# Optimization experiments

Measured on AMD Instinct MI355X. Metric: run time of the kernel, lower is better.

Reference implementation:

```python
import jax, jax.numpy as jnp
import numpy as np

B, S, D = 4, 2048, 2048
E = 64           # num_experts
TOPK = 2         # num_experts_per_token


def setup_inputs() -> dict:
    key = jax.random.key(0)
    k1, k2, k3 = jax.random.split(key, 3)
    x_real = jax.random.normal(k1, (B, S, D), dtype=jnp.float32)
    x_imag = jax.random.normal(k2, (B, S, D), dtype=jnp.float32)
    # flax Dense: kernel [in_features, out_features] with lecun_normal-ish scale
    W = jax.random.normal(k3, (2 * D, E), dtype=jnp.float32) / np.sqrt(2.0 * D)
    b = jnp.zeros((E,), dtype=jnp.float32)
    return {"x_real": x_real, "x_imag": x_imag, "W": W, "b": b}


def reference(x_real, x_imag, W, b):
    # amp = |x|, phase = angle(x) for x = x_real + i*x_imag
    amp = jnp.hypot(x_real, x_imag)                 # [B,S,D]
    phase = jnp.arctan2(x_imag, x_real)             # [B,S,D]
    routing_input = jnp.concatenate([amp, phase], axis=-1)  # [B,S,2D]
    scores = jnp.einsum('bsf,fe->bse', routing_input, W) + b  # [B,S,E]
    probs = jax.nn.softmax(scores, axis=-1)
    top_k_probs, top_k_indices = jax.lax.top_k(probs, TOPK)   # [B,S,K]
    top_k_probs = top_k_probs / jnp.sum(top_k_probs, axis=-1, keepdims=True)
    return (top_k_probs, top_k_indices)
```

## Files before the change

### kernel.cpp

```cpp
#include <hip/hip_runtime.h>
#include <math.h>

#define NTOK 8192
#define DD   2048
#define EE   64
#define STRIP 16
#define NKH 8
#define DSLICE (DD/NKH)
#define NCH (DSLICE/32)
#define PROB_N (NTOK*2)
#define F_SSTRIDE (128*4*64*8)

typedef __bf16 bf16x8 __attribute__((ext_vector_type(8)));
typedef float  f32x4  __attribute__((ext_vector_type(4)));
typedef unsigned int u32x4 __attribute__((ext_vector_type(4)));

__device__ __forceinline__ void tsplit3(float x, unsigned short& h1,
                                        unsigned short& h2, unsigned short& h3) {
    const unsigned u = __builtin_bit_cast(unsigned, x);
    h1 = (unsigned short)(u >> 16);
    const float f1 = __builtin_bit_cast(float, u & 0xFFFF0000u);
    const float r1 = x - f1;
    const unsigned v = __builtin_bit_cast(unsigned, r1);
    h2 = (unsigned short)(v >> 16);
    const float f2 = __builtin_bit_cast(float, v & 0xFFFF0000u);
    const float r2 = r1 - f2;
    h3 = (unsigned short)(__builtin_bit_cast(unsigned, r2) >> 16);
}

__device__ __forceinline__ float fast_atan2f(float y, float x) {
    const float ax = __builtin_fabsf(x), ay = __builtin_fabsf(y);
    const float hi = fmaxf(ax, ay), lo = fminf(ax, ay);
    const bool  big = lo > 0.4142135679721832f * hi;
    const float num = big ? (lo - hi) : lo;
    const float den = big ? (lo + hi) : hi;
    float rc = __builtin_amdgcn_rcpf(den);
    rc = rc * fmaf(-den, rc, 2.0f);
    const float z  = num * rc;
    const float z2 = z * z;
    float p = fmaf(z2, 8.05374449538e-2f, -1.38776856032e-1f);
    p = fmaf(z2, p, 1.99777106478e-1f);
    p = fmaf(z2, p, -3.33329491539e-1f);
    float r = fmaf(z * z2, p, z);
    r = r + (big ? 0.78539816339744830962f : 0.0f);
    r = (ay > ax) ? (1.57079632679489661923f - r) : r;
    r = (x < 0.0f) ? (3.14159265358979323846f - r) : r;
    return copysignf(r, y);
}

__device__ __forceinline__ unsigned packhi(float a, float b) {
    return __builtin_amdgcn_perm(__builtin_bit_cast(unsigned, b),
                                 __builtin_bit_cast(unsigned, a), 0x07060302u);
}

__device__ __forceinline__ void split_planes(const float* v, bf16x8& o1,
                                             bf16x8& o2, bf16x8& o3) {
    u32x4 P1, P2, P3;
    #pragma unroll
    for (int p = 0; p < 4; ++p) {
        const float a = v[2 * p], b = v[2 * p + 1];
        const float f1a = __builtin_bit_cast(float, __builtin_bit_cast(unsigned, a) & 0xFFFF0000u);
        const float f1b = __builtin_bit_cast(float, __builtin_bit_cast(unsigned, b) & 0xFFFF0000u);
        const float r1a = a - f1a, r1b = b - f1b;
        const float f2a = __builtin_bit_cast(float, __builtin_bit_cast(unsigned, r1a) & 0xFFFF0000u);
        const float f2b = __builtin_bit_cast(float, __builtin_bit_cast(unsigned, r1b) & 0xFFFF0000u);
        const float r2a = r1a - f2a, r2b = r1b - f2b;
        P1[p] = packhi(a, b);
        P2[p] = packhi(r1a, r1b);
        P3[p] = packhi(r2a, r2b);
    }
    o1 = __builtin_bit_cast(bf16x8, P1);
    o2 = __builtin_bit_cast(bf16x8, P2);
    o3 = __builtin_bit_cast(bf16x8, P3);
}

__global__ __launch_bounds__(256) void wsplit(const float* __restrict__ W,
                                              unsigned short* __restrict__ F) {
    const int g  = blockIdx.x * 256 + threadIdx.x;
    const int e  = g & 63;
    const int q  = g >> 6;
    const int d0 = q * 4;
    const int nt = e >> 4;
    const int k  = d0 & 31;
    const int lane = (k >> 3) * 16 + (e & 15);
    const int j0 = k & 7;
    const int ck = 2 * (d0 >> 5);

    unsigned short ah[3][4], ph[3][4];
    #pragma unroll
    for (int i = 0; i < 4; ++i) {
        tsplit3(W[(size_t)(d0 + i) * EE + e],      ah[0][i], ah[1][i], ah[2][i]);
        tsplit3(W[(size_t)(DD + d0 + i) * EE + e], ph[0][i], ph[1][i], ph[2][i]);
    }
    #pragma unroll
    for (int s = 0; s < 3; ++s) {
        ushort4 va = make_ushort4(ah[s][0], ah[s][1], ah[s][2], ah[s][3]);
        ushort4 vp = make_ushort4(ph[s][0], ph[s][1], ph[s][2], ph[s][3]);
        *(ushort4*)&F[(size_t)(((s * 128 + ck)     * 4 + nt) * 64 + lane) * 8 + j0] = va;
        *(ushort4*)&F[(size_t)(((s * 128 + ck + 1) * 4 + nt) * 64 + lane) * 8 + j0] = vp;
    }
}

__global__ __launch_bounds__(512, 4) void gemm_topk(
    const float* __restrict__ xr, const float* __restrict__ xi,
    const unsigned short* __restrict__ F, const float* __restrict__ bias,
    float* __restrict__ out)
{
    __shared__ float score8[NKH][STRIP][EE];
    __shared__ float scoreF[STRIP][EE];

    const int tid  = threadIdx.x;
    const int wv   = tid >> 6;
    const int lane = tid & 63;
    const int fm   = lane & 15;
    const int fq   = lane >> 4;
    const int t0   = blockIdx.x * STRIP;

    const float* prx = xr + (size_t)(t0 + fm) * DD + wv * DSLICE + fq * 8;
    const float* pix = xi + (size_t)(t0 + fm) * DD + wv * DSLICE + fq * 8;
    const unsigned short* bs0 = F + (size_t)(wv * NCH * 2) * 4 * 512 + lane * 8;
    const unsigned short* bs1 = bs0 + F_SSTRIDE;
    const unsigned short* bs2 = bs0 + 2 * F_SSTRIDE;

    f32x4 acc[4];
    #pragma unroll
    for (int n = 0; n < 4; ++n) acc[n] = (f32x4){0.f, 0.f, 0.f, 0.f};

    float4 cr0 = *(const float4*)(prx);
    float4 cr1 = *(const float4*)(prx + 4);
    float4 ci0 = *(const float4*)(pix);
    float4 ci1 = *(const float4*)(pix + 4);
    prx += 32; pix += 32;

    #pragma unroll 2
    for (int c = 0; c < NCH; ++c) {
        float4 nr0, nr1, ni0, ni1;
        if (c + 1 < NCH) {
            nr0 = *(const float4*)(prx);
            nr1 = *(const float4*)(prx + 4);
            ni0 = *(const float4*)(pix);
            ni1 = *(const float4*)(pix + 4);
            prx += 32; pix += 32;
        } else {
            nr0 = cr0; nr1 = cr1; ni0 = ci0; ni1 = ci1;
        }

        const float ar[8] = {cr0.x, cr0.y, cr0.z, cr0.w, cr1.x, cr1.y, cr1.z, cr1.w};
        const float ai[8] = {ci0.x, ci0.y, ci0.z, ci0.w, ci1.x, ci1.y, ci1.z, ci1.w};

        {
            bf16x8 b1[4], b2[4], b3[4];
            #pragma unroll
            for (int n = 0; n < 4; ++n) {
                b1[n] = *(const bf16x8*)(bs0 + n * 512);
                b2[n] = *(const bf16x8*)(bs1 + n * 512);
                b3[n] = *(const bf16x8*)(bs2 + n * 512);
            }
            float av[8];
            #pragma unroll
            for (int j = 0; j < 8; ++j)
                av[j] = sqrtf(fmaf(ar[j], ar[j], ai[j] * ai[j]));
            bf16x8 a1, a2, a3;
            split_planes(av, a1, a2, a3);
            #pragma unroll
            for (int n = 0; n < 4; ++n) {
                acc[n] = __builtin_amdgcn_mfma_f32_16x16x32_bf16(a1, b1[n], acc[n], 0, 0, 0);
                acc[n] = __builtin_amdgcn_mfma_f32_16x16x32_bf16(a1, b2[n], acc[n], 0, 0, 0);
                acc[n] = __builtin_amdgcn_mfma_f32_16x16x32_bf16(a2, b1[n], acc[n], 0, 0, 0);
                acc[n] = __builtin_amdgcn_mfma_f32_16x16x32_bf16(a1, b3[n], acc[n], 0, 0, 0);
                acc[n] = __builtin_amdgcn_mfma_f32_16x16x32_bf16(a2, b2[n], acc[n], 0, 0, 0);
                acc[n] = __builtin_amdgcn_mfma_f32_16x16x32_bf16(a3, b1[n], acc[n], 0, 0, 0);
            }
        }
        {
            bf16x8 b1[4], b2[4], b3[4];
            #pragma unroll
            for (int n = 0; n < 4; ++n) {
                b1[n] = *(const bf16x8*)(bs0 + (4 + n) * 512);
                b2[n] = *(const bf16x8*)(bs1 + (4 + n) * 512);
                b3[n] = *(const bf16x8*)(bs2 + (4 + n) * 512);
            }
            float pv[8];
            #pragma unroll
            for (int j = 0; j < 8; ++j)
                pv[j] = fast_atan2f(ai[j], ar[j]);
            bf16x8 a1, a2, a3;
            split_planes(pv, a1, a2, a3);
            #pragma unroll
            for (int n = 0; n < 4; ++n) {
                acc[n] = __builtin_amdgcn_mfma_f32_16x16x32_bf16(a1, b1[n], acc[n], 0, 0, 0);
                acc[n] = __builtin_amdgcn_mfma_f32_16x16x32_bf16(a1, b2[n], acc[n], 0, 0, 0);
                acc[n] = __builtin_amdgcn_mfma_f32_16x16x32_bf16(a2, b1[n], acc[n], 0, 0, 0);
                acc[n] = __builtin_amdgcn_mfma_f32_16x16x32_bf16(a1, b3[n], acc[n], 0, 0, 0);
                acc[n] = __builtin_amdgcn_mfma_f32_16x16x32_bf16(a2, b2[n], acc[n], 0, 0, 0);
                acc[n] = __builtin_amdgcn_mfma_f32_16x16x32_bf16(a3, b1[n], acc[n], 0, 0, 0);
            }
        }
        bs0 += 8 * 512; bs1 += 8 * 512; bs2 += 8 * 512;
        cr0 = nr0; cr1 = nr1; ci0 = ni0; ci1 = ni1;
    }

    #pragma unroll
    for (int n = 0; n < 4; ++n)
        #pragma unroll
        for (int r = 0; r < 4; ++r)
            score8[wv][fq * 4 + r][n * 16 + fm] = acc[n][r];
    __syncthreads();

    #pragma unroll
    for (int rep = 0; rep < 2; ++rep) {
        const int p = tid + rep * 512;
        const int tok = p >> 6, e = p & 63;
        float s = bias[e];
        #pragma unroll
        for (int w = 0; w < NKH; ++w) s += score8[w][tok][e];
        scoreF[tok][e] = s;
    }
    __syncthreads();

    #pragma unroll
    for (int rep = 0; rep < 2; ++rep) {
        const int tok = wv + rep * 8;
        float v1 = scoreF[tok][lane], v2 = -INFINITY;
        int   i1 = lane, i2 = 64;
        #pragma unroll
        for (int off = 1; off < 64; off <<= 1) {
            const float ov1 = __shfl_xor(v1, off, 64);
            const int   oi1 = __shfl_xor(i1, off, 64);
            const float ov2 = __shfl_xor(v2, off, 64);
            const int   oi2 = __shfl_xor(i2, off, 64);
            const bool b1 = (ov1 > v1) || (ov1 == v1 && oi1 < i1);
            const float n1 = b1 ? ov1 : v1;  const int ni1 = b1 ? oi1 : i1;
            const float c1 = b1 ? v1  : ov1; const int ci1 = b1 ? i1  : oi1;
            const float c2 = b1 ? ov2 : v2;  const int ci2 = b1 ? oi2 : i2;
            const bool b2 = (c1 > c2) || (c1 == c2 && ci1 < ci2);
            v1 = n1; i1 = ni1;
            v2 = b2 ? c1 : c2; i2 = b2 ? ci1 : ci2;
        }
        if (lane == 0) {
            const int t = t0 + tok;
            const float z  = expf(v2 - v1);
            const float p1 = 1.0f / (1.0f + z);
            const float p2 = z / (1.0f + z);
            out[(size_t)t * 2 + 0] = p1;
            out[(size_t)t * 2 + 1] = p2;
            out[PROB_N + (size_t)t * 2 + 0] = (float)i1;
            out[PROB_N + (size_t)t * 2 + 1] = (float)i2;
        }
    }
}

extern "C" void kernel_launch(void* const* d_in, const int* in_sizes, int n_in,
                              void* d_out, int out_size, void* d_ws, size_t ws_size,
                              hipStream_t stream) {
    const float* xr = (const float*)d_in[0];
    const float* xi = (const float*)d_in[1];
    const float* W  = (const float*)d_in[2];
    const float* b  = (const float*)d_in[3];
    float* out = (float*)d_out;
    unsigned short* F = (unsigned short*)d_ws;

    wsplit<<<128, 256, 0, stream>>>(W, F);
    gemm_topk<<<NTOK / STRIP, 512, 0, stream>>>(xr, xi, F, b, out);
}
```

Measured before the change: 187.6 us.

## Split K across two blocks per token strip with atomic score reduction

The GEMM kernel now splits the feature dimension across two blocks per 16-token strip, which doubles the grid and raises the occupancy hint. Partial scores are combined with global atomicAdd into a zeroed workspace buffer. A separate finalize kernel then does the top-2 softmax selection. The inner loop also drops the register double-buffering of x loads and interleaves the B fragment loads with the MFMAs. The aim is more parallelism and latency hiding, at the cost of an extra launch, atomic traffic and an 8192x64 score round-trip through memory.

After: 196.9 us. 1.05x slower.

```diff
diff --git a/kernel.cpp b/kernel.cpp
--- a/kernel.cpp
+++ b/kernel.cpp
@@ -4,10 +4,11 @@
 #define NTOK 8192
 #define DD   2048
 #define EE   64
-#define STRIP 16
-#define NKH 8
-#define DSLICE (DD/NKH)
-#define NCH (DSLICE/32)
+#define TSTRIP 16
+#define NKW 8
+#define KSPL 2
+#define DW 128
+#define NCH (DW/32)
 #define PROB_N (NTOK*2)
 #define F_SSTRIDE (128*4*64*8)
 
@@ -75,7 +76,8 @@
 }
 
 __global__ __launch_bounds__(256) void wsplit(const float* __restrict__ W,
-                                              unsigned short* __restrict__ F) {
+                                              unsigned short* __restrict__ F,
+                                              float* __restrict__ score) {
     const int g  = blockIdx.x * 256 + threadIdx.x;
     const int e  = g & 63;
     const int q  = g >> 6;
@@ -99,105 +101,80 @@
         *(ushort4*)&F[(size_t)(((s * 128 + ck)     * 4 + nt) * 64 + lane) * 8 + j0] = va;
         *(ushort4*)&F[(size_t)(((s * 128 + ck + 1) * 4 + nt) * 64 + lane) * 8 + j0] = vp;
     }
-}
-
-__global__ __launch_bounds__(512, 4) void gemm_topk(
+    float4* sz = (float4*)score;
+    #pragma unroll
+    for (int r = 0; r < 4; ++r)
+        sz[(size_t)g * 4 + r] = make_float4(0.f, 0.f, 0.f, 0.f);
+}
+
+__global__ __launch_bounds__(512, 8) void gemm_mfma(
     const float* __restrict__ xr, const float* __restrict__ xi,
-    const unsigned short* __restrict__ F, const float* __restrict__ bias,
-    float* __restrict__ out)
+    const unsigned short* __restrict__ F, float* __restrict__ score)
 {
-    __shared__ float score8[NKH][STRIP][EE];
-    __shared__ float scoreF[STRIP][EE];
+    __shared__ float score8[NKW][TSTRIP][EE];
 
     const int tid  = threadIdx.x;
     const int wv   = tid >> 6;
     const int lane = tid & 63;
     const int fm   = lane & 15;
     const int fq   = lane >> 4;
-    const int t0   = blockIdx.x * STRIP;
-
-    const float* prx = xr + (size_t)(t0 + fm) * DD + wv * DSLICE + fq * 8;
-    const float* pix = xi + (size_t)(t0 + fm) * DD + wv * DSLICE + fq * 8;
-    const unsigned short* bs0 = F + (size_t)(wv * NCH * 2) * 4 * 512 + lane * 8;
-    const unsigned short* bs1 = bs0 + F_SSTRIDE;
-    const unsigned short* bs2 = bs0 + 2 * F_SSTRIDE;
+    const int ks   = blockIdx.x & (KSPL - 1);
+    const int t0   = (blockIdx.x >> 1) * TSTRIP;
+    const int dbase = ks * (DD / KSPL) + wv * DW;
+
+    const float* prx = xr + (size_t)(t0 + fm) * DD + dbase + fq * 8;
+    const float* pix = xi + (size_t)(t0 + fm) * DD + dbase + fq * 8;
+    const unsigned short* bs = F + (size_t)(2 * (dbase >> 5)) * 2048 + lane * 8;
 
     f32x4 acc[4];
     #pragma unroll
     for (int n = 0; n < 4; ++n) acc[n] = (f32x4){0.f, 0.f, 0.f, 0.f};
 
-    float4 cr0 = *(const float4*)(prx);
-    float4 cr1 = *(const float4*)(prx + 4);
-    float4 ci0 = *(const float4*)(pix);
-    float4 ci1 = *(const float4*)(pix + 4);
-    prx += 32; pix += 32;
-
-    #pragma unroll 2
     for (int c = 0; c < NCH; ++c) {
-        float4 nr0, nr1, ni0, ni1;
-        if (c + 1 < NCH) {
-            nr0 = *(const float4*)(prx);
-            nr1 = *(const float4*)(prx + 4);
-            ni0 = *(const float4*)(pix);
-            ni1 = *(const float4*)(pix + 4);
-            prx += 32; pix += 32;
-        } else {
-            nr0 = cr0; nr1 = cr1; ni0 = ci0; ni1 = ci1;
+        const float4 vr0 = *(const float4*)(prx);
+        const float4 vr1 = *(const float4*)(prx + 4);
+        const float4 vi0 = *(const float4*)(pix);
+        const float4 vi1 = *(const float4*)(pix + 4);
+        prx += 32; pix += 32;
+
+        const float ar[8] = {vr0.x, vr0.y, vr0.z, vr0.w, vr1.x, vr1.y, vr1.z, vr1.w};
+        const float ai[8] = {vi0.x, vi0.y, vi0.z, vi0.w, vi1.x, vi1.y, vi1.z, vi1.w};
+
+        float av[8], pv[8];
+        #pragma unroll
+        for (int j = 0; j < 8; ++j) {
+            av[j] = __builtin_amdgcn_sqrtf(fmaf(ar[j], ar[j], ai[j] * ai[j]));
+            pv[j] = fast_atan2f(ai[j], ar[j]);
         }
-
-        const float ar[8] = {cr0.x, cr0.y, cr0.z, cr0.w, cr1.x, cr1.y, cr1.z, cr1.w};
-        const float ai[8] = {ci0.x, ci0.y, ci0.z, ci0.w, ci1.x, ci1.y, ci1.z, ci1.w};
-
-        {
-            bf16x8 b1[4], b2[4], b3[4];
-            #pragma unroll
-            for (int n = 0; n < 4; ++n) {
-                b1[n] = *(const bf16x8*)(bs0 + n * 512);
-                b2[n] = *(const bf16x8*)(bs1 + n * 512);
-                b3[n] = *(const bf16x8*)(bs2 + n * 512);
-            }
-            float av[8];
-            #pragma unroll
-            for (int j = 0; j < 8; ++j)
-                av[j] = sqrtf(fmaf(ar[j], ar[j], ai[j] * ai[j]));
-            bf16x8 a1, a2, a3;
-            split_planes(av, a1, a2, a3);
-            #pragma unroll
-            for (int n = 0; n < 4; ++n) {
-                acc[n] = __builtin_amdgcn_mfma_f32_16x16x32_bf16(a1, b1[n], acc[n], 0, 0, 0);
-                acc[n] = __builtin_amdgcn_mfma_f32_16x16x32_bf16(a1, b2[n], acc[n], 0, 0, 0);
-                acc[n] = __builtin_amdgcn_mfma_f32_16x16x32_bf16(a2, b1[n], acc[n], 0, 0, 0);
-                acc[n] = __builtin_amdgcn_mfma_f32_16x16x32_bf16(a1, b3[n], acc[n], 0, 0, 0);
-                acc[n] = __builtin_amdgcn_mfma_f32_16x16x32_bf16(a2, b2[n], acc[n], 0, 0, 0);
-                acc[n] = __builtin_amdgcn_mfma_f32_16x16x32_bf16(a3, b1[n], acc[n], 0, 0, 0);
-            }
+        bf16x8 a1, a2, a3, p1, p2, p3;
+        split_planes(av, a1, a2, a3);
+        split_planes(pv, p1, p2, p3);
+
+        #pragma unroll
+        for (int n = 0; n < 4; ++n) {
+            const bf16x8 b1 = *(const bf16x8*)(bs + n * 512);
+            const bf16x8 b2 = *(const bf16x8*)(bs + n * 512 + F_SSTRIDE);
+            const bf16x8 b3 = *(const bf16x8*)(bs + n * 512 + 2 * F_SSTRIDE);
+            acc[n] = __builtin_amdgcn_mfma_f32_16x16x32_bf16(a1, b1, acc[n], 0, 0, 0);
+            acc[n] = __builtin_amdgcn_mfma_f32_16x16x32_bf16(a1, b2, acc[n], 0, 0, 0);
+            acc[n] = __builtin_amdgcn_mfma_f32_16x16x32_bf16(a2, b1, acc[n], 0, 0, 0);
+            acc[n] = __builtin_amdgcn_mfma_f32_16x16x32_bf16(a1, b3, acc[n], 0, 0, 0);
+            acc[n] = __builtin_amdgcn_mfma_f32_16x16x32_bf16(a2, b2, acc[n], 0, 0, 0);
+            acc[n] = __builtin_amdgcn_mfma_f32_16x16x32_bf16(a3, b1, acc[n], 0, 0, 0);
         }
-        {
-            bf16x8 b1[4], b2[4], b3[4];
-            #pragma unroll
-            for (int n = 0; n < 4; ++n) {
-                b1[n] = *(const bf16x8*)(bs0 + (4 + n) * 512);
-                b2[n] = *(const bf16x8*)(bs1 + (4 + n) * 512);
-                b3[n] = *(const bf16x8*)(bs2 + (4 + n) * 512);
-            }
-            float pv[8];
-            #pragma unroll
-            for (int j = 0; j < 8; ++j)
-                pv[j] = fast_atan2f(ai[j], ar[j]);
-            bf16x8 a1, a2, a3;
-            split_planes(pv, a1, a2, a3);
-            #pragma unroll
-            for (int n = 0; n < 4; ++n) {
-                acc[n] = __builtin_amdgcn_mfma_f32_16x16x32_bf16(a1, b1[n], acc[n], 0, 0, 0);
-                acc[n] = __builtin_amdgcn_mfma_f32_16x16x32_bf16(a1, b2[n], acc[n], 0, 0, 0);
-                acc[n] = __builtin_amdgcn_mfma_f32_16x16x32_bf16(a2, b1[n], acc[n], 0, 0, 0);
-                acc[n] = __builtin_amdgcn_mfma_f32_16x16x32_bf16(a1, b3[n], acc[n], 0, 0, 0);
-                acc[n] = __builtin_amdgcn_mfma_f32_16x16x32_bf16(a2, b2[n], acc[n], 0, 0, 0);
-                acc[n] = __builtin_amdgcn_mfma_f32_16x16x32_bf16(a3, b1[n], acc[n], 0, 0, 0);
-            }
+        #pragma unroll
+        for (int n = 0; n < 4; ++n) {
+            const bf16x8 b1 = *(const bf16x8*)(bs + 2048 + n * 512);
+            const bf16x8 b2 = *(const bf16x8*)(bs + 2048 + n * 512 + F_SSTRIDE);
+            const bf16x8 b3 = *(const bf16x8*)(bs + 2048 + n * 512 + 2 * F_SSTRIDE);
+            acc[n] = __builtin_amdgcn_mfma_f32_16x16x32_bf16(p1, b1, acc[n], 0, 0, 0);
+            acc[n] = __builtin_amdgcn_mfma_f32_16x16x32_bf16(p1, b2, acc[n], 0, 0, 0);
+            acc[n] = __builtin_amdgcn_mfma_f32_16x16x32_bf16(p2, b1, acc[n], 0, 0, 0);
+            acc[n] = __builtin_amdgcn_mfma_f32_16x16x32_bf16(p1, b3, acc[n], 0, 0, 0);
+            acc[n] = __builtin_amdgcn_mfma_f32_16x16x32_bf16(p2, b2, acc[n], 0, 0, 0);
+            acc[n] = __builtin_amdgcn_mfma_f32_16x16x32_bf16(p3, b1, acc[n], 0, 0, 0);
         }
-        bs0 += 8 * 512; bs1 += 8 * 512; bs2 += 8 * 512;
-        cr0 = nr0; cr1 = nr1; ci0 = ni0; ci1 = ni1;
+        bs += 4096;
     }
 
     #pragma unroll
@@ -211,42 +188,49 @@
     for (int rep = 0; rep < 2; ++rep) {
         const int p = tid + rep * 512;
         const int tok = p >> 6, e = p & 63;
-        float s = bias[e];
-        #pragma unroll
-        for (int w = 0; w < NKH; ++w) s += score8[w][tok][e];
-        scoreF[tok][e] = s;
-    }
-    __syncthreads();
-
-    #pragma unroll
-    for (int rep = 0; rep < 2; ++rep) {
-        const int tok = wv + rep * 8;
-        float v1 = scoreF[tok][lane], v2 = -INFINITY;
-        int   i1 = lane, i2 = 64;
-        #pragma unroll
-        for (int off = 1; off < 64; off <<= 1) {
-            const float ov1 = __shfl_xor(v1, off, 64);
-            const int   oi1 = __shfl_xor(i1, off, 64);
-            const float ov2 = __shfl_xor(v2, off, 64);
-            const int   oi2 = __shfl_xor(i2, off, 64);
-            const bool b1 = (ov1 > v1) || (ov1 == v1 && oi1 < i1);
-            const float n1 = b1 ? ov1 : v1;  const int ni1 = b1 ? oi1 : i1;
-            const float c1 = b1 ? v1  : ov1; const int ci1 = b1 ? i1  : oi1;
-            const float c2 = b1 ? ov2 : v2;  const int ci2 = b1 ? oi2 : i2;
-            const bool b2 = (c1 > c2) || (c1 == c2 && ci1 < ci2);
-            v1 = n1; i1 = ni1;
-            v2 = b2 ? c1 : c2; i2 = b2 ? ci1 : ci2;
-        }
-        if (lane == 0) {
-            const int t = t0 + tok;
-            const float z  = expf(v2 - v1);
-            const float p1 = 1.0f / (1.0f + z);
-            const float p2 = z / (1.0f + z);
-            out[(size_t)t * 2 + 0] = p1;
-            out[(size_t)t * 2 + 1] = p2;
-            out[PROB_N + (size_t)t * 2 + 0] = (float)i1;
-            out[PROB_N + (size_t)t * 2 + 1] = (float)i2;
-        }
+        float s = score8[0][tok][e];
+        #pragma unroll
+        for (int w = 1; w < NKW; ++w) s += score8[w][tok][e];
+        atomicAdd(&score[(size_t)(t0 + tok) * EE + e], s);
+    }
+}
+
+__global__ __launch_bounds__(256) void finalize_topk(
+    const float* __restrict__ score, const float* __restrict__ bias,
+    float* __restrict__ out)
+{
+    const int tid  = threadIdx.x;
+    const int lane = tid & 63;
+    const int w    = tid >> 6;
+    const int t    = blockIdx.x * 4 + w;
+
+    float v1 = bias[lane] + score[(size_t)t * EE + lane];
+    float v2 = -INFINITY;
+    int   i1 = lane, i2 = 64;
+
+    #pragma unroll
+    for (int off = 1; off < 64; off <<= 1) {
+        const float ov1 = __shfl_xor(v1, off, 64);
+        const int   oi1 = __shfl_xor(i1, off, 64);
+        const float ov2 = __shfl_xor(v2, off, 64);
+        const int   oi2 = __shfl_xor(i2, off, 64);
+        const bool b1 = (ov1 > v1) || (ov1 == v1 && oi1 < i1);
+        const float n1 = b1 ? ov1 : v1;  const int ni1 = b1 ? oi1 : i1;
+        const float c1 = b1 ? v1  : ov1; const int ci1 = b1 ? i1  : oi1;
+        const float c2 = b1 ? ov2 : v2;  const int ci2 = b1 ? oi2 : i2;
+        const bool b2 = (c1 > c2) || (c1 == c2 && ci1 < ci2);
+        v1 = n1; i1 = ni1;
+        v2 = b2 ? c1 : c2; i2 = b2 ? ci1 : ci2;
+    }
+
+    if (lane == 0) {
+        const float z  = expf(v2 - v1);
+        const float p1 = 1.0f / (1.0f + z);
+        const float p2 = z / (1.0f + z);
+        out[(size_t)t * 2 + 0] = p1;
+        out[(size_t)t * 2 + 1] = p2;
+        out[PROB_N + (size_t)t * 2 + 0] = (float)i1;
+        out[PROB_N + (size_t)t * 2 + 1] = (float)i2;
     }
 }
 
@@ -258,8 +242,11 @@
     const float* W  = (const float*)d_in[2];
     const float* b  = (const float*)d_in[3];
     float* out = (float*)d_out;
-    unsigned short* F = (unsigned short*)d_ws;
-
-    wsplit<<<128, 256, 0, stream>>>(W, F);
-    gemm_topk<<<NTOK / STRIP, 512, 0, stream>>>(xr, xi, F, b, out);
-}
+
+    float* score = (float*)d_ws;
+    unsigned short* F = (unsigned short*)((char*)d_ws + (size_t)NTOK * EE * 4);
+
+    wsplit<<<128, 256, 0, stream>>>(W, F, score);
+    gemm_mfma<<<(NTOK / TSTRIP) * KSPL, 512, 0, stream>>>(xr, xi, F, score);
+    finalize_topk<<<NTOK / 4, 256, 0, stream>>>(score, b, out);
+}
```
